# Performance work log

Measured on AMD Instinct MI355X. Metric: run time of the kernel, lower is better.

Reference implementation:

```python
import jax, jax.numpy as jnp
import numpy as np

B, S, D, H = 1024, 20000, 256, 4  # batch, num_symbols, embed_dim, n_heads
Dh = D // H


def setup_inputs() -> dict:
    key = jax.random.key(0)
    ks = jax.random.split(key, 6)
    symbol_activations = jax.random.randint(ks[0], (B, S), 0, 2, dtype=jnp.int32)
    neural_context = jax.random.normal(ks[1], (B, D), dtype=jnp.float32)
    scale = 1.0 / np.sqrt(D)
    embed_table = jax.random.normal(ks[2], (S, D), dtype=jnp.float32)  # s2n_embed.weight
    in_proj_w = jax.random.normal(ks[3], (3 * D, D), dtype=jnp.float32) * scale  # MHA in_proj
    in_proj_b = jnp.zeros((3 * D,), dtype=jnp.float32)
    out_proj_w = jax.random.normal(ks[4], (D, D), dtype=jnp.float32) * scale
    out_proj_b = jnp.zeros((D,), dtype=jnp.float32)
    return dict(symbol_activations=symbol_activations, neural_context=neural_context,
                embed_table=embed_table, in_proj_w=in_proj_w, in_proj_b=in_proj_b,
                out_proj_w=out_proj_w, out_proj_b=out_proj_b)


def reference(symbol_activations, neural_context, embed_table,
              in_proj_w, in_proj_b, out_proj_w, out_proj_b):
    # symbolic_to_neural(symbol_activations, neural_context):
    # per-sample attention of the 1-token context over the active symbol embeddings.
    # Expressed as one dense masked attention over all S symbols (identical math).
    Wq, Wk, Wv = in_proj_w[:D], in_proj_w[D:2 * D], in_proj_w[2 * D:]
    bq, bk, bv = in_proj_b[:D], in_proj_b[D:2 * D], in_proj_b[2 * D:]

    q = neural_context @ Wq.T + bq                      # [B, D]
    k = embed_table @ Wk.T + bk                         # [S, D] (shared across batch)
    v = embed_table @ Wv.T + bv                         # [S, D]

    qh = q.reshape(B, H, Dh)
    kh = k.reshape(S, H, Dh)
    vh = v.reshape(S, H, Dh)

    scores = jnp.einsum('bhd,shd->bhs', qh, kh) / np.sqrt(Dh)  # [B, H, S]
    mask = symbol_activations > 0                                # [B, S]
    neg = jnp.asarray(-1e9, scores.dtype)
    scores = jnp.where(mask[:, None, :], scores, neg)
    attn = jax.nn.softmax(scores, axis=-1)
    ctxh = jnp.einsum('bhs,shd->bhd', attn, vh)                  # [B, H, Dh]

    # zero-active fallback: torch attends to mean(embed_table) as the single key;
    # softmax over one key == 1, so the head output is its value projection.
    mean_emb = embed_table.mean(axis=0)                          # [D]
    v_mean = (mean_emb @ Wv.T + bv).reshape(H, Dh)               # [H, Dh]
    has_active = mask.any(axis=-1)[:, None, None]                # [B, 1, 1]
    ctxh = jnp.where(has_active, ctxh, v_mean[None])

    out = ctxh.reshape(B, D) @ out_proj_w.T + out_proj_b         # [B, D]
    return out
```

## Files before the change

### kernel.cpp

```cpp
#include <hip/hip_runtime.h>

typedef unsigned int uint_t;
typedef unsigned long long u64;
typedef unsigned short u16;
typedef __attribute__((ext_vector_type(4))) float f32x4;
typedef __attribute__((ext_vector_type(16))) float f32x16;
typedef __attribute__((ext_vector_type(8))) __bf16 bf16x8;

#define S_TOT 20000
#define S_LD  20032
#define B_TOT 1024
#define NHEAD 4
#define NSPLIT 32
#define NCHUNK 313
#define NGRP   79

__device__ __forceinline__ u16 f2bf(float x) {
  uint_t u = __builtin_bit_cast(uint_t, x);
  u += 0x7FFFu + ((u >> 16) & 1u);
  return (u16)(u >> 16);
}

__device__ __forceinline__ uint_t cvtpk(float lo, float hi) {
  uint_t r;
  asm("v_cvt_pk_bf16_f32 %0, %1, %2" : "=v"(r) : "v"(lo), "v"(hi));
  return r;
}

__device__ __forceinline__ bf16x8 ld_frag(const void* p) {
  return __builtin_bit_cast(bf16x8, *(const uint4*)p);
}

__device__ __forceinline__ void gload_lds16(const void* g, void* l) {
  __builtin_amdgcn_global_load_lds((const __attribute__((address_space(1))) unsigned int*)g,
                                   (__attribute__((address_space(3))) unsigned int*)l, 16, 0, 0);
}

__global__ void pack_conv(const int* __restrict__ act, u64* __restrict__ pmT,
                          const float* __restrict__ ipw, const float* __restrict__ opw,
                          const float* __restrict__ nc, const float* __restrict__ emb,
                          u16* __restrict__ wqkv, u16* __restrict__ wout, u16* __restrict__ ncb,
                          u16* __restrict__ embb, u16* __restrict__ vt) {
  const int bx = blockIdx.x;
  if (bx < 5512) {
    const float* src; u16* dst;
    if (bx < 512) {
      int i = (bx * 256 + threadIdx.x) * 4;
      if (i < 196608)      { src = ipw + i;            dst = wqkv + i; }
      else if (i < 262144) { src = opw + (i - 196608); dst = wout + (i - 196608); }
      else                 { src = nc  + (i - 262144); dst = ncb  + (i - 262144); }
    } else {
      int i = ((bx - 512) * 256 + threadIdx.x) * 4;
      src = emb + i; dst = embb + i;
    }
    float4 v = *(const float4*)src;
    uint2 o;
    o.x = f2bf(v.x) | ((uint_t)f2bf(v.y) << 16);
    o.y = f2bf(v.z) | ((uint_t)f2bf(v.w) << 16);
    *(uint2*)dst = o;
    return;
  }
  if (bx < 25736) {
    const int gw = (bx - 5512) * 4 + (threadIdx.x >> 6);
    const int lane = threadIdx.x & 63;
    const int row = gw / NGRP, gi = gw - row * NGRP;
    const int s = gi * 256 + lane * 4;
    int4 v = make_int4(0, 0, 0, 0);
    if (s < S_TOT) v = *(const int4*)(act + (size_t)row * S_TOT + s);
    uint_t nib = (v.x > 0 ? 1u : 0u) | (v.y > 0 ? 2u : 0u) |
                 (v.z > 0 ? 4u : 0u) | (v.w > 0 ? 8u : 0u);
    u64 v64 = (u64)nib << (4 * (lane & 15));
    v64 |= __shfl_xor(v64, 1);
    v64 |= __shfl_xor(v64, 2);
    v64 |= __shfl_xor(v64, 4);
    v64 |= __shfl_xor(v64, 8);
    if ((lane & 15) == 0)
      pmT[(size_t)(gi * 4 + (lane >> 4)) * B_TOT + row] = v64;
    return;
  }
  int i = (bx - 25736) * 256 + threadIdx.x;
  int d = i >> 5, j = i & 31;
  vt[(size_t)d * S_LD + S_TOT + j] = 0;
}

__launch_bounds__(256)
__global__ void gemm_bt(const u16* __restrict__ A, const u16* __restrict__ W,
                        const float* __restrict__ bias, int M,
                        float* __restrict__ of) {
  __shared__ __align__(16) u16 sA[64][40];
  __shared__ __align__(16) u16 sW[64][40];
  const int t = threadIdx.x;
  const int w = t >> 6, lane = t & 63, lr = lane & 15, lg = lane >> 4;
  const int m0 = blockIdx.x * 64, n0 = blockIdx.y * 64;
  const int r = t >> 2, kc = (t & 3) * 8;
  f32x4 acc[4] = {};
  int ga = m0 + r; if (ga > M - 1) ga = M - 1;
  const u16* ap = A + (size_t)ga * 256;
  const u16* wp = W + (size_t)(n0 + r) * 256;
  for (int k0 = 0; k0 < 256; k0 += 32) {
    *(uint4*)&sA[r][kc] = *(const uint4*)(ap + k0 + kc);
    *(uint4*)&sW[r][kc] = *(const uint4*)(wp + k0 + kc);
    __syncthreads();
    bf16x8 af = ld_frag(&sA[16 * w + lr][lg * 8]);
#pragma unroll
    for (int nf = 0; nf < 4; nf++) {
      bf16x8 bfr = ld_frag(&sW[16 * nf + lr][lg * 8]);
      acc[nf] = __builtin_amdgcn_mfma_f32_16x16x32_bf16(af, bfr, acc[nf], 0, 0, 0);
    }
    __syncthreads();
  }
  const int rbase = m0 + 16 * w + lg * 4;
#pragma unroll
  for (int nf = 0; nf < 4; nf++) {
    const int n = n0 + nf * 16 + lr;
    const float bi = bias[n];
#pragma unroll
    for (int g = 0; g < 4; g++)
      if (rbase + g < M) of[(size_t)(rbase + g) * 256 + n] = acc[nf][g] + bi;
  }
}

__launch_bounds__(256, 3)
__global__ void gemm_kvq(const u16* __restrict__ embb, const u16* __restrict__ ncb,
                         const u16* __restrict__ wqkv, const float* __restrict__ ipb,
                         u16* __restrict__ kb, u16* __restrict__ vtb, u16* __restrict__ qb,
                         float qsc) {
  const int by = blockIdx.y;
  const int qmode = (by >= 8);
  if (qmode && blockIdx.x >= 8) return;
  __shared__ __align__(16) u16 sA[2][128][64];
  __shared__ __align__(16) u16 sW[2][64][64];
  const int t = threadIdx.x, w = t >> 6, lane = t & 63;
  const int q5 = lane & 31, hi = lane >> 5;
  const int wr = w >> 1, wc = w & 1;
  const int m0 = blockIdx.x * 128;
  const int M = qmode ? B_TOT : S_TOT;
  const u16* A = qmode ? ncb : embb;
  const int wrow0 = qmode ? (by - 8) * 64 : 256 + by * 64;
  const u16* W = wqkv + (size_t)wrow0 * 256;
  const float* bias = ipb + wrow0;

  auto stage = [&](int buf, int k0) {
#pragma unroll
    for (int j = 0; j < 4; j++) {
      int c = j * 256 + w * 64 + lane;
      int row = c >> 3, slot = c & 7;
      int gm = m0 + row; if (gm > M - 1) gm = M - 1;
      gload_lds16(A + (size_t)gm * 256 + k0 + ((slot ^ (row & 7)) * 8),
                  &sA[buf][0][0] + (size_t)(j * 256 + w * 64) * 8);
    }
#pragma unroll
    for (int j = 0; j < 2; j++) {
      int c = j * 256 + w * 64 + lane;
      int row = c >> 3, slot = c & 7;
      gload_lds16(W + (size_t)row * 256 + k0 + ((slot ^ (row & 7)) * 8),
                  &sW[buf][0][0] + (size_t)(j * 256 + w * 64) * 8);
    }
  };

  f32x16 acc[2] = {{}, {}};
  stage(0, 0);
  __syncthreads();
  for (int ks = 0; ks < 4; ks++) {
    const int buf = ks & 1;
    if (ks < 3) stage(buf ^ 1, (ks + 1) * 64);
#pragma unroll
    for (int k4 = 0; k4 < 4; k4++) {
      const int rowW = wc * 32 + q5;
      bf16x8 wf = ld_frag(&sW[buf][rowW][((2 * k4 + hi) ^ (rowW & 7)) * 8]);
#pragma unroll
      for (int blk = 0; blk < 2; blk++) {
        const int rowA = wr * 64 + blk * 32 + q5;
        bf16x8 af = ld_frag(&sA[buf][rowA][((2 * k4 + hi) ^ (rowA & 7)) * 8]);
        acc[blk] = __builtin_amdgcn_mfma_f32_32x32x16_bf16(af, wf, acc[blk], 0, 0, 0);
      }
    }
    __syncthreads();
  }
  const int nl = wc * 32 + q5;
  const float bi = bias[nl];
  if (qmode) {
    const int n = (by - 8) * 64 + nl;
#pragma unroll
    for (int blk = 0; blk < 2; blk++)
#pragma unroll
      for (int r = 0; r < 16; r++) {
        int mrow = m0 + wr * 64 + blk * 32 + (r & 3) + 8 * (r >> 2) + 4 * hi;
        if (mrow < B_TOT) qb[(size_t)mrow * 256 + n] = f2bf((acc[blk][r] + bi) * qsc);
      }
    return;
  }
  const int n = by * 64 + nl;
  if (n < 256) {
#pragma unroll
    for (int blk = 0; blk < 2; blk++)
#pragma unroll
      for (int r = 0; r < 16; r++) {
        int mrow = m0 + wr * 64 + blk * 32 + (r & 3) + 8 * (r >> 2) + 4 * hi;
        if (mrow < S_TOT) kb[(size_t)mrow * 256 + n] = f2bf(acc[blk][r] + bi);
      }
  } else {
    const int vr = n - 256;
#pragma unroll
    for (int blk = 0; blk < 2; blk++)
#pragma unroll
      for (int g = 0; g < 4; g++) {
        int mb = m0 + wr * 64 + blk * 32 + 8 * g + 4 * hi;
        u16 b4[4];
#pragma unroll
        for (int j = 0; j < 4; j++) b4[j] = f2bf(acc[blk][4 * g + j] + bi);
        if (mb + 3 < S_TOT) {
          uint2 p2; p2.x = b4[0] | ((uint_t)b4[1] << 16); p2.y = b4[2] | ((uint_t)b4[3] << 16);
          *(uint2*)&vtb[(size_t)vr * S_LD + mb] = p2;
        } else {
#pragma unroll
          for (int j = 0; j < 4; j++) if (mb + j < S_TOT) vtb[(size_t)vr * S_LD + mb + j] = b4[j];
        }
      }
  }
}

__launch_bounds__(256)
__attribute__((amdgpu_waves_per_eu(4, 4)))
__global__ void attn_k(const u16* __restrict__ qb, const u16* __restrict__ kb,
                       const u16* __restrict__ vt, const u64* __restrict__ pmT,
                       float* __restrict__ pc, float* __restrict__ pl) {
  __shared__ __align__(16) u16 sK[2][64][64];
  __shared__ __align__(16) u16 sV[2][64][64];
  const int t = threadIdx.x;
  const int w = t >> 6, lane = t & 63;
  const int q5 = lane & 31, hi = lane >> 5;
  const int si = blockIdx.x, bt = blockIdx.y, h = blockIdx.z;
  const int qrow = bt * 128 + w * 32 + q5;

  bf16x8 qf[4];
#pragma unroll
  for (int kc = 0; kc < 4; kc++)
    qf[kc] = ld_frag(qb + (size_t)qrow * 256 + h * 64 + kc * 16 + hi * 8);

  f32x16 ctx[2] = {{}, {}};
  f32x16 accl = {};
  const uint_t one2 = 0x3F803F80u;
  uint4 onesw; onesw.x = one2; onesw.y = one2; onesw.z = one2; onesw.w = one2;
  const bf16x8 onesf = __builtin_bit_cast(bf16x8, onesw);

  const int rg = w * 16 + (lane >> 3);
  const int c16 = (lane & 7) ^ ((lane >> 3) & 7);
  const u16* kst = kb + (size_t)(si * 64 + rg) * 256 + h * 64 + c16 * 8;
  const u16* vst = vt + (size_t)(h * 64 + rg) * S_LD + si * 64 + c16 * 8;
  const u64* mptr = pmT + (size_t)si * B_TOT + qrow;
  const size_t KSTEP = (size_t)NSPLIT * 64 * 256;
  const int    VSTEP = NSPLIT * 64;
  const size_t MSTEP = (size_t)NSPLIT * B_TOT;

  auto stage = [&](int buf) {
    gload_lds16(kst,            &sK[buf][w * 16][0]);
    gload_lds16(kst + 8 * 256,  &sK[buf][w * 16 + 8][0]);
    gload_lds16(vst,            &sV[buf][w * 16][0]);
    gload_lds16(vst + 8 * S_LD, &sV[buf][w * 16 + 8][0]);
    kst += KSTEP; vst += VSTEP;
  };

  auto body = [&](int buf) {
    const u64 m64 = *mptr; mptr += MSTEP;
    f32x16 sc0 = {}, sc1 = {};
#pragma unroll
    for (int kc = 0; kc < 4; kc++) {
      const int slot = ((2 * kc + hi) ^ (q5 & 7)) * 8;
      bf16x8 ka0 = ld_frag(&sK[buf][q5][slot]);
      bf16x8 ka1 = ld_frag(&sK[buf][32 + q5][slot]);
      sc0 = __builtin_amdgcn_mfma_f32_32x32x16_bf16(ka0, qf[kc], sc0, 0, 0, 0);
      sc1 = __builtin_amdgcn_mfma_f32_32x32x16_bf16(ka1, qf[kc], sc1, 0, 0, 0);
    }
    const uint_t mw0 = (uint_t)(m64 >> (4 * hi));
    const uint_t mw1 = (uint_t)(m64 >> (32 + 4 * hi));
#pragma unroll
    for (int r = 0; r < 16; r++) {
      const uint_t bsel = 1u << ((r & 3) + 8 * (r >> 2));
      sc0[r] = (mw0 & bsel) ? sc0[r] : -1e9f;
      sc1[r] = (mw1 & bsel) ? sc1[r] : -1e9f;
    }
    uint2 pk[2][4];
#pragma unroll
    for (int j = 0; j < 4; j++) {
      float a0 = exp2f(sc0[4 * j + 0]), a1 = exp2f(sc0[4 * j + 1]);
      float a2 = exp2f(sc0[4 * j + 2]), a3 = exp2f(sc0[4 * j + 3]);
      float b0 = exp2f(sc1[4 * j + 0]), b1 = exp2f(sc1[4 * j + 1]);
      float b2 = exp2f(sc1[4 * j + 2]), b3 = exp2f(sc1[4 * j + 3]);
      pk[0][j].x = cvtpk(a0, a1); pk[0][j].y = cvtpk(a2, a3);
      pk[1][j].x = cvtpk(b0, b1); pk[1][j].y = cvtpk(b2, b3);
    }
    const u16* Vrow = &sV[buf][q5][0];
#pragma unroll
    for (int u = 0; u < 4; u++) {
      const int b = u >> 1, v = u & 1;
      uint_t a0 = pk[b][2 * v].x,     a1 = pk[b][2 * v].y;
      uint_t b0 = pk[b][2 * v + 1].x, b1 = pk[b][2 * v + 1].y;
      asm("v_permlane32_swap_b32 %0, %1" : "+v"(a0), "+v"(b0));
      asm("v_permlane32_swap_b32 %0, %1" : "+v"(a1), "+v"(b1));
      uint4 bw; bw.x = a0; bw.y = a1; bw.z = b0; bw.w = b1;
      bf16x8 pfrag = __builtin_bit_cast(bf16x8, bw);
      const int slot = ((2 * u + hi) ^ (q5 & 7)) * 8;
      bf16x8 va0 = ld_frag(Vrow + slot);
      bf16x8 va1 = ld_frag(Vrow + 32 * 64 + slot);
      ctx[0] = __builtin_amdgcn_mfma_f32_32x32x16_bf16(va0, pfrag, ctx[0], 0, 0, 0);
      ctx[1] = __builtin_amdgcn_mfma_f32_32x32x16_bf16(va1, pfrag, ctx[1], 0, 0, 0);
      accl   = __builtin_amdgcn_mfma_f32_32x32x16_bf16(onesf, pfrag, accl, 0, 0, 0);
    }
  };

  stage(0);
  __syncthreads();
  int ci = si;
  for (;;) {
    if (ci + NSPLIT < NCHUNK) stage(1);
    body(0);
    __syncthreads();
    ci += NSPLIT;
    if (ci >= NCHUNK) break;
    if (ci + NSPLIT < NCHUNK) stage(0);
    body(1);
    __syncthreads();
    ci += NSPLIT;
    if (ci >= NCHUNK) break;
  }

  size_t obase = (((size_t)si * B_TOT + qrow) * NHEAD + h) * 64;
#pragma unroll
  for (int dc = 0; dc < 2; dc++)
#pragma unroll
    for (int r = 0; r < 16; r++) {
      int d = dc * 32 + (r & 3) + 8 * (r >> 2) + 4 * hi;
      pc[obase + d] = ctx[dc][r];
    }
  if (lane < 32)
    pl[((size_t)si * B_TOT + qrow) * NHEAD + h] = accl[0];
}

__global__ void combine_k(const float* __restrict__ pc, const float* __restrict__ pl,
                          const u16* __restrict__ vtb, u16* __restrict__ ctxb) {
  const int b = blockIdx.x, t = threadIdx.x;
  const int h = t >> 6, d = t & 63;
  float L = 0.f, a = 0.f;
#pragma unroll 8
  for (int si = 0; si < NSPLIT; si++) {
    size_t base = ((size_t)si * B_TOT + b) * NHEAD + h;
    L += pl[base];
    a += pc[(base << 6) + d];
  }
  float vmv = 0.f;
  if (__builtin_expect(L == 0.f, 0)) {
    float s = 0.f;
    for (int c = 0; c < 2504; c++) {
      bf16x8 v = ld_frag(vtb + (size_t)(h * 64 + d) * S_LD + c * 8);
#pragma unroll
      for (int i = 0; i < 8; i++) s += (float)v[i];
    }
    vmv = s * (1.0f / 20000.0f);
  }
  float r = (L == 0.f) ? vmv : (a / L);
  ctxb[(size_t)b * 256 + t] = f2bf(r);
}

extern "C" void kernel_launch(void* const* d_in, const int* in_sizes, int n_in,
                              void* d_out, int out_size, void* d_ws, size_t ws_size,
                              hipStream_t stream) {
  const int*   act = (const int*)d_in[0];
  const float* nc  = (const float*)d_in[1];
  const float* emb = (const float*)d_in[2];
  const float* ipw = (const float*)d_in[3];
  const float* ipb = (const float*)d_in[4];
  const float* opw = (const float*)d_in[5];
  const float* opb = (const float*)d_in[6];
  float* out = (float*)d_out;
  char* ws = (char*)d_ws;

  size_t off = 0;
  auto alloc = [&](size_t bytes) { size_t r0 = off; off = (off + bytes + 255) & ~(size_t)255; return r0; };
  u16*   wqkv = (u16*)(ws + alloc(768 * 256 * 2));
  u16*   wout = (u16*)(ws + alloc(256 * 256 * 2));
  u16*   ncb  = (u16*)(ws + alloc((size_t)B_TOT * 256 * 2));
  u16*   qb   = (u16*)(ws + alloc((size_t)B_TOT * 256 * 2));
  u16*   kbuf = (u16*)(ws + alloc((size_t)S_LD * 256 * 2));
  u16*   vtb  = (u16*)(ws + alloc((size_t)256 * S_LD * 2));
  float* pl   = (float*)(ws + alloc((size_t)NSPLIT * B_TOT * NHEAD * 4));
  u16*   ctxb = (u16*)(ws + alloc((size_t)B_TOT * 256 * 2));
  u64*   pmT  = (u64*)(ws + alloc((size_t)NGRP * 4 * B_TOT * 8));
  size_t ubase = off;
  u16*   embb = (u16*)(ws + ubase);
  float* pc   = (float*)(ws + ubase);

  const float QSC = 0.125f * 1.44269504089f;

  pack_conv<<<25768, 256, 0, stream>>>(act, pmT, ipw, opw, nc, emb, wqkv, wout, ncb, embb, vtb);
  gemm_kvq<<<dim3(157, 12), 256, 0, stream>>>(embb, ncb, wqkv, ipb, kbuf, vtb, qb, QSC);
  attn_k<<<dim3(NSPLIT, B_TOT / 128, NHEAD), 256, 0, stream>>>(qb, kbuf, vtb, pmT, pc, pl);
  combine_k<<<B_TOT, 256, 0, stream>>>(pc, pl, vtb, ctxb);
  gemm_bt<<<dim3(16, 4), 256, 0, stream>>>(ctxb, wout, opb, B_TOT, out);
}
```

Measured before the change: 107.0 us.

## Co-schedule mask bit-packing with K/V/Q projection GEMM in one interleaved launch

Moves the activation-mask bit-packing out of the conversion kernel and into the projection GEMM kernel. Blocks are interleaved 3:4 between GEMM work and packing work, so the memory-bound mask read overlaps the MFMA-bound projection. Each packing wave now handles 8 groups with a one-ahead prefetched load instead of 1. The aim is to hide the large int32 mask read behind compute, at the cost of more complex block indexing and some wasted idle blocks.

```diff
diff --git a/kernel.cpp b/kernel.cpp
--- a/kernel.cpp
+++ b/kernel.cpp
@@ -36,11 +36,10 @@
                                    (__attribute__((address_space(3))) unsigned int*)l, 16, 0, 0);
 }
 
-__global__ void pack_conv(const int* __restrict__ act, u64* __restrict__ pmT,
-                          const float* __restrict__ ipw, const float* __restrict__ opw,
-                          const float* __restrict__ nc, const float* __restrict__ emb,
-                          u16* __restrict__ wqkv, u16* __restrict__ wout, u16* __restrict__ ncb,
-                          u16* __restrict__ embb, u16* __restrict__ vt) {
+__global__ void conv_k(const float* __restrict__ ipw, const float* __restrict__ opw,
+                       const float* __restrict__ nc, const float* __restrict__ emb,
+                       u16* __restrict__ wqkv, u16* __restrict__ wout, u16* __restrict__ ncb,
+                       u16* __restrict__ embb, u16* __restrict__ vt) {
   const int bx = blockIdx.x;
   if (bx < 5512) {
     const float* src; u16* dst;
@@ -60,27 +59,148 @@
     *(uint2*)dst = o;
     return;
   }
-  if (bx < 25736) {
-    const int gw = (bx - 5512) * 4 + (threadIdx.x >> 6);
-    const int lane = threadIdx.x & 63;
-    const int row = gw / NGRP, gi = gw - row * NGRP;
-    const int s = gi * 256 + lane * 4;
-    int4 v = make_int4(0, 0, 0, 0);
-    if (s < S_TOT) v = *(const int4*)(act + (size_t)row * S_TOT + s);
-    uint_t nib = (v.x > 0 ? 1u : 0u) | (v.y > 0 ? 2u : 0u) |
-                 (v.z > 0 ? 4u : 0u) | (v.w > 0 ? 8u : 0u);
-    u64 v64 = (u64)nib << (4 * (lane & 15));
-    v64 |= __shfl_xor(v64, 1);
-    v64 |= __shfl_xor(v64, 2);
-    v64 |= __shfl_xor(v64, 4);
-    v64 |= __shfl_xor(v64, 8);
-    if ((lane & 15) == 0)
-      pmT[(size_t)(gi * 4 + (lane >> 4)) * B_TOT + row] = v64;
-    return;
-  }
-  int i = (bx - 25736) * 256 + threadIdx.x;
+  int i = (bx - 5512) * 256 + threadIdx.x;
   int d = i >> 5, j = i & 31;
   vt[(size_t)d * S_LD + S_TOT + j] = 0;
+}
+
+__launch_bounds__(256, 3)
+__global__ void packkvq(const int* __restrict__ act, u64* __restrict__ pmT,
+                        const u16* __restrict__ embb, const u16* __restrict__ ncb,
+                        const u16* __restrict__ wqkv, const float* __restrict__ ipb,
+                        u16* __restrict__ kb, u16* __restrict__ vtb, u16* __restrict__ qb,
+                        float qsc) {
+  __shared__ __align__(16) u16 sA[2][128][64];
+  __shared__ __align__(16) u16 sW[2][64][64];
+  const int bx = blockIdx.x;
+  const int r7 = bx % 7, q7 = bx / 7;
+  const int t = threadIdx.x;
+
+  if (r7 >= 3) {
+    const int pki = q7 * 4 + (r7 - 3);
+    const int lane = t & 63;
+    int gw = (pki * 4 + (t >> 6)) * 8;
+    int row = gw / NGRP, gi = gw - row * NGRP;
+    int s = gi * 256 + lane * 4;
+    int4 nxt = (s < S_TOT) ? *(const int4*)(act + (size_t)row * S_TOT + s)
+                           : make_int4(0, 0, 0, 0);
+    int rowc = row, gic = gi;
+#pragma unroll
+    for (int it = 0; it < 8; it++) {
+      int4 cur = nxt;
+      int rows = rowc, gis = gic;
+      if (it < 7) {
+        gic++; if (gic == NGRP) { gic = 0; rowc++; }
+        int s2 = gic * 256 + lane * 4;
+        nxt = (s2 < S_TOT) ? *(const int4*)(act + (size_t)rowc * S_TOT + s2)
+                           : make_int4(0, 0, 0, 0);
+      }
+      uint_t nib = (cur.x > 0 ? 1u : 0u) | (cur.y > 0 ? 2u : 0u) |
+                   (cur.z > 0 ? 4u : 0u) | (cur.w > 0 ? 8u : 0u);
+      u64 v64 = (u64)nib << (4 * (lane & 15));
+      v64 |= __shfl_xor(v64, 1);
+      v64 |= __shfl_xor(v64, 2);
+      v64 |= __shfl_xor(v64, 4);
+      v64 |= __shfl_xor(v64, 8);
+      if ((lane & 15) == 0)
+        pmT[(size_t)(gis * 4 + (lane >> 4)) * B_TOT + rows] = v64;
+    }
+    return;
+  }
+
+  const int kvi = q7 * 3 + r7;
+  if (kvi >= 1884) return;
+  const int kx = kvi % 157, ky = kvi / 157;
+  const int qmode = (ky >= 8);
+  if (qmode && kx >= 8) return;
+  const int w = t >> 6, lane = t & 63;
+  const int q5 = lane & 31, hi = lane >> 5;
+  const int wr = w >> 1, wc = w & 1;
+  const int m0 = kx * 128;
+  const int M = qmode ? B_TOT : S_TOT;
+  const u16* A = qmode ? ncb : embb;
+  const int wrow0 = qmode ? (ky - 8) * 64 : 256 + ky * 64;
+  const u16* W = wqkv + (size_t)wrow0 * 256;
+  const float* bias = ipb + wrow0;
+
+  auto stage = [&](int buf, int k0) {
+#pragma unroll
+    for (int j = 0; j < 4; j++) {
+      int c = j * 256 + w * 64 + lane;
+      int row = c >> 3, slot = c & 7;
+      int gm = m0 + row; if (gm > M - 1) gm = M - 1;
+      gload_lds16(A + (size_t)gm * 256 + k0 + ((slot ^ (row & 7)) * 8),
+                  &sA[buf][0][0] + (size_t)(j * 256 + w * 64) * 8);
+    }
+#pragma unroll
+    for (int j = 0; j < 2; j++) {
+      int c = j * 256 + w * 64 + lane;
+      int row = c >> 3, slot = c & 7;
+      gload_lds16(W + (size_t)row * 256 + k0 + ((slot ^ (row & 7)) * 8),
+                  &sW[buf][0][0] + (size_t)(j * 256 + w * 64) * 8);
+    }
+  };
+
+  f32x16 acc[2] = {{}, {}};
+  stage(0, 0);
+  __syncthreads();
+  for (int ks = 0; ks < 4; ks++) {
+    const int buf = ks & 1;
+    if (ks < 3) stage(buf ^ 1, (ks + 1) * 64);
+#pragma unroll
+    for (int k4 = 0; k4 < 4; k4++) {
+      const int rowW = wc * 32 + q5;
+      bf16x8 wf = ld_frag(&sW[buf][rowW][((2 * k4 + hi) ^ (rowW & 7)) * 8]);
+#pragma unroll
+      for (int blk = 0; blk < 2; blk++) {
+        const int rowA = wr * 64 + blk * 32 + q5;
+        bf16x8 af = ld_frag(&sA[buf][rowA][((2 * k4 + hi) ^ (rowA & 7)) * 8]);
+        acc[blk] = __builtin_amdgcn_mfma_f32_32x32x16_bf16(af, wf, acc[blk], 0, 0, 0);
+      }
+    }
+    __syncthreads();
+  }
+  const int nl = wc * 32 + q5;
+  const float bi = bias[nl];
+  if (qmode) {
+    const int n = (ky - 8) * 64 + nl;
+#pragma unroll
+    for (int blk = 0; blk < 2; blk++)
+#pragma unroll
+      for (int r = 0; r < 16; r++) {
+        int mrow = m0 + wr * 64 + blk * 32 + (r & 3) + 8 * (r >> 2) + 4 * hi;
+        if (mrow < B_TOT) qb[(size_t)mrow * 256 + n] = f2bf((acc[blk][r] + bi) * qsc);
+      }
+    return;
+  }
+  const int n = ky * 64 + nl;
+  if (n < 256) {
+#pragma unroll
+    for (int blk = 0; blk < 2; blk++)
+#pragma unroll
+      for (int r = 0; r < 16; r++) {
+        int mrow = m0 + wr * 64 + blk * 32 + (r & 3) + 8 * (r >> 2) + 4 * hi;
+        if (mrow < S_TOT) kb[(size_t)mrow * 256 + n] = f2bf(acc[blk][r] + bi);
+      }
+  } else {
+    const int vr = n - 256;
+#pragma unroll
+    for (int blk = 0; blk < 2; blk++)
+#pragma unroll
+      for (int g = 0; g < 4; g++) {
+        int mb = m0 + wr * 64 + blk * 32 + 8 * g + 4 * hi;
+        u16 b4[4];
+#pragma unroll
+        for (int j = 0; j < 4; j++) b4[j] = f2bf(acc[blk][4 * g + j] + bi);
+        if (mb + 3 < S_TOT) {
+          uint2 p2; p2.x = b4[0] | ((uint_t)b4[1] << 16); p2.y = b4[2] | ((uint_t)b4[3] << 16);
+          *(uint2*)&vtb[(size_t)vr * S_LD + mb] = p2;
+        } else {
+#pragma unroll
+          for (int j = 0; j < 4; j++) if (mb + j < S_TOT) vtb[(size_t)vr * S_LD + mb + j] = b4[j];
+        }
+      }
+  }
 }
 
 __launch_bounds__(256)
@@ -120,106 +240,6 @@
   }
 }
 
-__launch_bounds__(256, 3)
-__global__ void gemm_kvq(const u16* __restrict__ embb, const u16* __restrict__ ncb,
-                         const u16* __restrict__ wqkv, const float* __restrict__ ipb,
-                         u16* __restrict__ kb, u16* __restrict__ vtb, u16* __restrict__ qb,
-                         float qsc) {
-  const int by = blockIdx.y;
-  const int qmode = (by >= 8);
-  if (qmode && blockIdx.x >= 8) return;
-  __shared__ __align__(16) u16 sA[2][128][64];
-  __shared__ __align__(16) u16 sW[2][64][64];
-  const int t = threadIdx.x, w = t >> 6, lane = t & 63;
-  const int q5 = lane & 31, hi = lane >> 5;
-  const int wr = w >> 1, wc = w & 1;
-  const int m0 = blockIdx.x * 128;
-  const int M = qmode ? B_TOT : S_TOT;
-  const u16* A = qmode ? ncb : embb;
-  const int wrow0 = qmode ? (by - 8) * 64 : 256 + by * 64;
-  const u16* W = wqkv + (size_t)wrow0 * 256;
-  const float* bias = ipb + wrow0;
-
-  auto stage = [&](int buf, int k0) {
-#pragma unroll
-    for (int j = 0; j < 4; j++) {
-      int c = j * 256 + w * 64 + lane;
-      int row = c >> 3, slot = c & 7;
-      int gm = m0 + row; if (gm > M - 1) gm = M - 1;
-      gload_lds16(A + (size_t)gm * 256 + k0 + ((slot ^ (row & 7)) * 8),
-                  &sA[buf][0][0] + (size_t)(j * 256 + w * 64) * 8);
-    }
-#pragma unroll
-    for (int j = 0; j < 2; j++) {
-      int c = j * 256 + w * 64 + lane;
-      int row = c >> 3, slot = c & 7;
-      gload_lds16(W + (size_t)row * 256 + k0 + ((slot ^ (row & 7)) * 8),
-                  &sW[buf][0][0] + (size_t)(j * 256 + w * 64) * 8);
-    }
-  };
-
-  f32x16 acc[2] = {{}, {}};
-  stage(0, 0);
-  __syncthreads();
-  for (int ks = 0; ks < 4; ks++) {
-    const int buf = ks & 1;
-    if (ks < 3) stage(buf ^ 1, (ks + 1) * 64);
-#pragma unroll
-    for (int k4 = 0; k4 < 4; k4++) {
-      const int rowW = wc * 32 + q5;
-      bf16x8 wf = ld_frag(&sW[buf][rowW][((2 * k4 + hi) ^ (rowW & 7)) * 8]);
-#pragma unroll
-      for (int blk = 0; blk < 2; blk++) {
-        const int rowA = wr * 64 + blk * 32 + q5;
-        bf16x8 af = ld_frag(&sA[buf][rowA][((2 * k4 + hi) ^ (rowA & 7)) * 8]);
-        acc[blk] = __builtin_amdgcn_mfma_f32_32x32x16_bf16(af, wf, acc[blk], 0, 0, 0);
-      }
-    }
-    __syncthreads();
-  }
-  const int nl = wc * 32 + q5;
-  const float bi = bias[nl];
-  if (qmode) {
-    const int n = (by - 8) * 64 + nl;
-#pragma unroll
-    for (int blk = 0; blk < 2; blk++)
-#pragma unroll
-      for (int r = 0; r < 16; r++) {
-        int mrow = m0 + wr * 64 + blk * 32 + (r & 3) + 8 * (r >> 2) + 4 * hi;
-        if (mrow < B_TOT) qb[(size_t)mrow * 256 + n] = f2bf((acc[blk][r] + bi) * qsc);
-      }
-    return;
-  }
-  const int n = by * 64 + nl;
-  if (n < 256) {
-#pragma unroll
-    for (int blk = 0; blk < 2; blk++)
-#pragma unroll
-      for (int r = 0; r < 16; r++) {
-        int mrow = m0 + wr * 64 + blk * 32 + (r & 3) + 8 * (r >> 2) + 4 * hi;
-        if (mrow < S_TOT) kb[(size_t)mrow * 256 + n] = f2bf(acc[blk][r] + bi);
-      }
-  } else {
-    const int vr = n - 256;
-#pragma unroll
-    for (int blk = 0; blk < 2; blk++)
-#pragma unroll
-      for (int g = 0; g < 4; g++) {
-        int mb = m0 + wr * 64 + blk * 32 + 8 * g + 4 * hi;
-        u16 b4[4];
-#pragma unroll
-        for (int j = 0; j < 4; j++) b4[j] = f2bf(acc[blk][4 * g + j] + bi);
-        if (mb + 3 < S_TOT) {
-          uint2 p2; p2.x = b4[0] | ((uint_t)b4[1] << 16); p2.y = b4[2] | ((uint_t)b4[3] << 16);
-          *(uint2*)&vtb[(size_t)vr * S_LD + mb] = p2;
-        } else {
-#pragma unroll
-          for (int j = 0; j < 4; j++) if (mb + j < S_TOT) vtb[(size_t)vr * S_LD + mb + j] = b4[j];
-        }
-      }
-  }
-}
-
 __launch_bounds__(256)
 __attribute__((amdgpu_waves_per_eu(4, 4)))
 __global__ void attn_k(const u16* __restrict__ qb, const u16* __restrict__ kb,
@@ -392,8 +412,8 @@
 
   const float QSC = 0.125f * 1.44269504089f;
 
-  pack_conv<<<25768, 256, 0, stream>>>(act, pmT, ipw, opw, nc, emb, wqkv, wout, ncb, embb, vtb);
-  gemm_kvq<<<dim3(157, 12), 256, 0, stream>>>(embb, ncb, wqkv, ipb, kbuf, vtb, qb, QSC);
+  conv_k<<<5544, 256, 0, stream>>>(ipw, opw, nc, emb, wqkv, wout, ncb, embb, vtb);
+  packkvq<<<7 * 632, 256, 0, stream>>>(act, pmT, embb, ncb, wqkv, ipb, kbuf, vtb, qb, QSC);
   attn_k<<<dim3(NSPLIT, B_TOT / 128, NHEAD), 256, 0, stream>>>(qb, kbuf, vtb, pmT, pc, pl);
   combine_k<<<B_TOT, 256, 0, stream>>>(pc, pl, vtb, ctxb);
   gemm_bt<<<dim3(16, 4), 256, 0, stream>>>(ctxb, wout, opb, B_TOT, out);
```

Result: slower. 109.3 us (+2.2%).
